# Kernel tuning notes

Hardware: AMD Instinct MI355X
Metric: run time of the kernel (lower is better)

The kernel has to match this reference:

```python
import jax, jax.numpy as jnp
import numpy as np

T, H, E, I = 16384, 2048, 16, 1408


def setup_inputs() -> dict:
    key = jax.random.key(0)
    k1, k2, k3, k4 = jax.random.split(key, 4)
    hidden_states = jax.random.normal(k1, (T, H), dtype=jnp.float32)
    router_logits = jax.random.normal(k2, (T, E), dtype=jnp.float32)
    # w13 = merged [gate; up] projection per expert: [E, 2*I, H] (w1 first, then w3)
    w13 = jax.random.normal(k3, (E, 2 * I, H), dtype=jnp.float32) * 0.02
    # w2 = down projection per expert: [E, H, I]
    w2 = jax.random.normal(k4, (E, H, I), dtype=jnp.float32) * 0.02
    return {
        "hidden_states": hidden_states,
        "router_logits": router_logits,
        "w13": w13,
        "w2": w2,
        "top_k": 2,
    }


def reference(hidden_states, router_logits, w13, w2, top_k):
    t, h = hidden_states.shape
    e = router_logits.shape[1]
    i = w2.shape[2]
    # softmax over experts, select top-k, renormalize selected weights
    probs = jax.nn.softmax(router_logits, axis=-1)                      # [T, E]
    topk_w, topk_ids = jax.lax.top_k(probs, top_k)                      # [T, K]
    topk_w = topk_w / jnp.sum(topk_w, axis=-1, keepdims=True)
    # dense combine weights, transposed to [E, T] for per-expert scan
    cw = jnp.zeros((t, e), probs.dtype).at[
        jnp.arange(t)[:, None], topk_ids
    ].add(topk_w).T                                                     # [E, T]

    def expert_step(out, inp):
        w13_e, w2_e, cw_e = inp                                         # [2I,H], [H,I], [T]
        g = hidden_states @ w13_e.T                                     # [T, 2I]
        act = jax.nn.silu(g[:, :i]) * g[:, i:]                          # SiLU-and-mul -> [T, I]
        y = act @ w2_e.T                                                # [T, H]
        return out + cw_e[:, None] * y, None

    out0 = jnp.zeros_like(hidden_states)
    out, _ = jax.lax.scan(expert_step, out0, (w13, w2, cw))
    return out
```

## Files before the change

kernel.cpp:

```cpp
#include <hip/hip_runtime.h>
#include <cstdio>
#include <cstdint>

#define T_TOK 16384
#define H_DIM 2048
#define E_NUM 16
#define I_DIM 1408
#define TWO_I 2816
#define PMAX  34816
#define MAXMT 272

typedef unsigned short ushort_t;
typedef __attribute__((ext_vector_type(8))) short bf16x8;
typedef __attribute__((ext_vector_type(4))) float f32x4;
typedef __attribute__((ext_vector_type(8))) unsigned short us8;

__device__ __forceinline__ ushort_t f2bf(float x) {
  union { float f; unsigned int u; } v; v.f = x;
  unsigned int r = v.u + 0x7fffu + ((v.u >> 16) & 1u);
  return (ushort_t)(r >> 16);
}

__device__ __forceinline__ float bf2f(ushort_t u) {
  union { unsigned int i; float f; } v; v.i = ((unsigned int)u) << 16; return v.f;
}

__device__ __forceinline__ void async_copy16(const void* g, void* l) {
  __builtin_amdgcn_global_load_lds(
      (const __attribute__((address_space(1))) unsigned int*)g,
      (__attribute__((address_space(3))) unsigned int*)l, 16, 0, 0);
}

__global__ void zero_small(int* counts, int* fill, int* ntl) {
  int i = threadIdx.x;
  if (i < E_NUM) { counts[i] = 0; fill[i] = 0; }
  if (i == 0) ntl[0] = 0;
}

__global__ void router_kernel(const float* __restrict__ logits,
                              int* __restrict__ tok_e, float* __restrict__ tok_w,
                              int* __restrict__ counts) {
  int t = blockIdx.x * 256 + threadIdx.x;
  if (t >= T_TOK) return;
  const float* lp = logits + (size_t)t * E_NUM;
  float b1 = -1e30f, b2 = -1e30f; int i1 = 0, i2 = 0;
#pragma unroll
  for (int e = 0; e < E_NUM; ++e) {
    float v = lp[e];
    if (v > b1) { b2 = b1; i2 = i1; b1 = v; i1 = e; }
    else if (v > b2) { b2 = v; i2 = e; }
  }
  float w1 = 1.f / (1.f + __expf(b2 - b1));
  tok_e[2 * t] = i1; tok_e[2 * t + 1] = i2;
  tok_w[2 * t] = w1; tok_w[2 * t + 1] = 1.f - w1;
  atomicAdd(&counts[i1], 1);
  atomicAdd(&counts[i2], 1);
}

__global__ void scan_kernel(const int* __restrict__ counts, int* __restrict__ base_e,
                            int* __restrict__ tile_expert, int* __restrict__ tile_base,
                            int* __restrict__ ntl) {
  if (threadIdx.x != 0) return;
  int base = 0, nt = 0;
  for (int e = 0; e < E_NUM; ++e) {
    base_e[e] = base;
    int c = counts[e];
    int tiles = (c + 127) >> 7;
    for (int ti = 0; ti < tiles; ++ti) { tile_expert[nt] = e; tile_base[nt] = base + ti * 128; ++nt; }
    base += tiles << 7;
  }
  ntl[0] = nt;
}

__global__ void slot_init_kernel(int* st, float* sw) {
  int i = blockIdx.x * 256 + threadIdx.x;
  if (i < PMAX) { st[i] = 0; sw[i] = 0.f; }
}

__global__ void scatter_kernel(const int* __restrict__ tok_e, const float* __restrict__ tok_w,
                               const int* __restrict__ base_e, int* __restrict__ fill,
                               int* __restrict__ st, float* __restrict__ sw,
                               int* __restrict__ tslot) {
  int t = blockIdx.x * 256 + threadIdx.x;
  if (t >= T_TOK) return;
#pragma unroll
  for (int k = 0; k < 2; ++k) {
    int e = tok_e[2 * t + k];
    int pos = atomicAdd(&fill[e], 1);
    int slot = base_e[e] + pos;
    st[slot] = t; sw[slot] = tok_w[2 * t + k];
    tslot[2 * t + k] = slot;
  }
}

__device__ __forceinline__ us8 pack8(float4 a, float4 b) {
  us8 r;
  r[0] = f2bf(a.x); r[1] = f2bf(a.y); r[2] = f2bf(a.z); r[3] = f2bf(a.w);
  r[4] = f2bf(b.x); r[5] = f2bf(b.y); r[6] = f2bf(b.z); r[7] = f2bf(b.w);
  return r;
}

__global__ void cvt_hidden(const float* __restrict__ src, ushort_t* __restrict__ dst) {
  size_t i8 = ((size_t)blockIdx.x * 256 + threadIdx.x) * 8;
  const float4* s = (const float4*)(src + i8);
  *(us8*)(dst + i8) = pack8(s[0], s[1]);
}

__global__ void cvt_w13(const float* __restrict__ src, ushort_t* __restrict__ dst) {
  size_t i8 = ((size_t)blockIdx.x * 256 + threadIdx.x) * 8;
  const size_t per_e = (size_t)TWO_I * H_DIM;
  int e = (int)(i8 / per_e);
  size_t rem = i8 - (size_t)e * per_e;
  int n = (int)(rem / H_DIM);
  int c = (int)(rem - (size_t)n * H_DIM);
  int np;
  if (n < I_DIM) np = ((n >> 4) << 5) + (n & 15);
  else { int m = n - I_DIM; np = ((m >> 4) << 5) + 16 + (m & 15); }
  const float4* s = (const float4*)(src + i8);
  *(us8*)(dst + (size_t)e * per_e + (size_t)np * H_DIM + c) = pack8(s[0], s[1]);
}

__global__ void cvt_w2(const float* __restrict__ src, ushort_t* __restrict__ dst) {
  size_t i8 = ((size_t)blockIdx.x * 256 + threadIdx.x) * 8;
  const float4* s = (const float4*)(src + i8);
  *(us8*)(dst + i8) = pack8(s[0], s[1]);
}

__global__ __launch_bounds__(256, 2) void gemm1_kernel(
    const ushort_t* __restrict__ Xb, const ushort_t* __restrict__ W13p,
    ushort_t* __restrict__ Act, const int* __restrict__ slot_token,
    const int* __restrict__ tile_expert, const int* __restrict__ tile_base,
    const int* __restrict__ ntl) {
  const int mt = blockIdx.y;
  if (mt >= ntl[0]) return;
  const int e = tile_expert[mt];
  const int slot0 = tile_base[mt];
  const int n0 = blockIdx.x * 128;

  __shared__ ushort_t As[128 * 64];
  __shared__ ushort_t Bs[128 * 64];
  __shared__ int toks[128];

  const int tid = threadIdx.x;
  if (tid < 128) toks[tid] = slot_token[slot0 + tid];
  __syncthreads();

  const int wave = tid >> 6;
  const int lane = tid & 63;
  const int r = lane & 15;
  const int q = lane >> 4;
  const int wm = wave >> 1;
  const int wn = wave & 1;

  const ushort_t* a_src[4];
  const ushort_t* b_src[4];
  ushort_t* a_dst[4];
  ushort_t* b_dst[4];
#pragma unroll
  for (int s = 0; s < 4; ++s) {
    int u = wave * 256 + s * 64 + lane;
    int m = u >> 3;
    int kc = (u & 7) ^ (m & 7);
    a_src[s] = Xb + (size_t)toks[m] * H_DIM + kc * 8;
    b_src[s] = W13p + (size_t)e * ((size_t)TWO_I * H_DIM) + (size_t)(n0 + m) * H_DIM + kc * 8;
    a_dst[s] = &As[(size_t)u * 8];
    b_dst[s] = &Bs[(size_t)u * 8];
  }

  int aoff[2][4], boff[2][4];
#pragma unroll
  for (int kh = 0; kh < 2; ++kh)
#pragma unroll
    for (int i = 0; i < 4; ++i) {
      int m = wm * 64 + i * 16 + r;
      aoff[kh][i] = (m * 8 + ((kh * 4 + q) ^ (r & 7))) * 8;
      int n = wn * 64 + i * 16 + r;
      boff[kh][i] = (n * 8 + ((kh * 4 + q) ^ (r & 7))) * 8;
    }

  f32x4 acc[4][4];
#pragma unroll
  for (int i = 0; i < 4; ++i)
#pragma unroll
    for (int j = 0; j < 4; ++j) acc[i][j] = (f32x4)(0.f);

  for (int kt = 0; kt < H_DIM / 64; ++kt) {
    const int koff = kt * 64;
#pragma unroll
    for (int s = 0; s < 4; ++s) {
      async_copy16(a_src[s] + koff, a_dst[s]);
      async_copy16(b_src[s] + koff, b_dst[s]);
    }
    __syncthreads();
#pragma unroll
    for (int kh = 0; kh < 2; ++kh) {
      bf16x8 af[4], bfr[4];
#pragma unroll
      for (int i = 0; i < 4; ++i) af[i] = *(const bf16x8*)&As[aoff[kh][i]];
#pragma unroll
      for (int j = 0; j < 4; ++j) bfr[j] = *(const bf16x8*)&Bs[boff[kh][j]];
#pragma unroll
      for (int i = 0; i < 4; ++i)
#pragma unroll
        for (int j = 0; j < 4; ++j)
          acc[i][j] = __builtin_amdgcn_mfma_f32_16x16x32_bf16(af[i], bfr[j], acc[i][j], 0, 0, 0);
    }
    __syncthreads();
  }

#pragma unroll
  for (int i = 0; i < 4; ++i) {
    const int row = slot0 + wm * 64 + i * 16 + q * 4;
#pragma unroll
    for (int jj = 0; jj < 2; ++jj) {
      const int g = 4 * (int)blockIdx.x + 2 * wn + jj;
      const int col = g * 16 + r;
      const f32x4 gv = acc[i][2 * jj];
      const f32x4 uv = acc[i][2 * jj + 1];
#pragma unroll
      for (int reg = 0; reg < 4; ++reg) {
        float gate = gv[reg];
        float a = gate / (1.f + __expf(-gate)) * uv[reg];
        Act[(size_t)(row + reg) * I_DIM + col] = f2bf(a);
      }
    }
  }
}

__global__ __launch_bounds__(256, 2) void gemm2_kernel(
    const ushort_t* __restrict__ Act, const ushort_t* __restrict__ W2b,
    ushort_t* __restrict__ Y, const float* __restrict__ slot_w,
    const int* __restrict__ tile_expert, const int* __restrict__ tile_base,
    const int* __restrict__ ntl) {
  const int mt = blockIdx.y;
  if (mt >= ntl[0]) return;
  const int e = tile_expert[mt];
  const int slot0 = tile_base[mt];
  const int n0 = blockIdx.x * 128;

  __shared__ ushort_t As[128 * 64];
  __shared__ ushort_t Bs[128 * 64];
  __shared__ float wgt[128];

  const int tid = threadIdx.x;
  if (tid < 128) wgt[tid] = slot_w[slot0 + tid];

  const int wave = tid >> 6;
  const int lane = tid & 63;
  const int r = lane & 15;
  const int q = lane >> 4;
  const int wm = wave >> 1;
  const int wn = wave & 1;

  const ushort_t* a_src[4];
  const ushort_t* b_src[4];
  ushort_t* a_dst[4];
  ushort_t* b_dst[4];
#pragma unroll
  for (int s = 0; s < 4; ++s) {
    int u = wave * 256 + s * 64 + lane;
    int m = u >> 3;
    int kc = (u & 7) ^ (m & 7);
    a_src[s] = Act + (size_t)(slot0 + m) * I_DIM + kc * 8;
    b_src[s] = W2b + (size_t)e * ((size_t)H_DIM * I_DIM) + (size_t)(n0 + m) * I_DIM + kc * 8;
    a_dst[s] = &As[(size_t)u * 8];
    b_dst[s] = &Bs[(size_t)u * 8];
  }

  int aoff[2][4], boff[2][4];
#pragma unroll
  for (int kh = 0; kh < 2; ++kh)
#pragma unroll
    for (int i = 0; i < 4; ++i) {
      int m = wm * 64 + i * 16 + r;
      aoff[kh][i] = (m * 8 + ((kh * 4 + q) ^ (r & 7))) * 8;
      int n = wn * 64 + i * 16 + r;
      boff[kh][i] = (n * 8 + ((kh * 4 + q) ^ (r & 7))) * 8;
    }

  f32x4 acc[4][4];
#pragma unroll
  for (int i = 0; i < 4; ++i)
#pragma unroll
    for (int j = 0; j < 4; ++j) acc[i][j] = (f32x4)(0.f);

  for (int kt = 0; kt < I_DIM / 64; ++kt) {
    const int koff = kt * 64;
#pragma unroll
    for (int s = 0; s < 4; ++s) {
      async_copy16(a_src[s] + koff, a_dst[s]);
      async_copy16(b_src[s] + koff, b_dst[s]);
    }
    __syncthreads();
#pragma unroll
    for (int kh = 0; kh < 2; ++kh) {
      bf16x8 af[4], bfr[4];
#pragma unroll
      for (int i = 0; i < 4; ++i) af[i] = *(const bf16x8*)&As[aoff[kh][i]];
#pragma unroll
      for (int j = 0; j < 4; ++j) bfr[j] = *(const bf16x8*)&Bs[boff[kh][j]];
#pragma unroll
      for (int i = 0; i < 4; ++i)
#pragma unroll
        for (int j = 0; j < 4; ++j)
          acc[i][j] = __builtin_amdgcn_mfma_f32_16x16x32_bf16(af[i], bfr[j], acc[i][j], 0, 0, 0);
    }
    __syncthreads();
  }

#pragma unroll
  for (int i = 0; i < 4; ++i) {
#pragma unroll
    for (int reg = 0; reg < 4; ++reg) {
      const int rl = wm * 64 + i * 16 + q * 4 + reg;
      const float w = wgt[rl];
      ushort_t* yrow = Y + (size_t)(slot0 + rl) * H_DIM;
#pragma unroll
      for (int j = 0; j < 4; ++j) {
        const int col = n0 + wn * 64 + j * 16 + r;
        yrow[col] = f2bf(w * acc[i][j][reg]);
      }
    }
  }
}

__global__ __launch_bounds__(256) void combine_kernel(
    const ushort_t* __restrict__ Y, const int* __restrict__ tslot,
    float* __restrict__ Out) {
  const int t = blockIdx.x;
  const int c = threadIdx.x * 8;
  const int s1 = tslot[2 * t];
  const int s2 = tslot[2 * t + 1];
  const us8 y1 = *(const us8*)(Y + (size_t)s1 * H_DIM + c);
  const us8 y2 = *(const us8*)(Y + (size_t)s2 * H_DIM + c);
  float4 o0, o1;
  o0.x = bf2f(y1[0]) + bf2f(y2[0]);
  o0.y = bf2f(y1[1]) + bf2f(y2[1]);
  o0.z = bf2f(y1[2]) + bf2f(y2[2]);
  o0.w = bf2f(y1[3]) + bf2f(y2[3]);
  o1.x = bf2f(y1[4]) + bf2f(y2[4]);
  o1.y = bf2f(y1[5]) + bf2f(y2[5]);
  o1.z = bf2f(y1[6]) + bf2f(y2[6]);
  o1.w = bf2f(y1[7]) + bf2f(y2[7]);
  float4* dst = (float4*)(Out + (size_t)t * H_DIM + c);
  dst[0] = o0;
  dst[1] = o1;
}

extern "C" void kernel_launch(void* const* d_in, const int* in_sizes, int n_in,
                              void* d_out, int out_size, void* d_ws, size_t ws_size,
                              hipStream_t stream) {
  const float* hidden = (const float*)d_in[0];
  const float* logits = (const float*)d_in[1];
  const float* w13    = (const float*)d_in[2];
  const float* w2     = (const float*)d_in[3];
  float* out = (float*)d_out;
  char* ws = (char*)d_ws;

  const size_t SZ_HID = (size_t)T_TOK * H_DIM * 2;
  const size_t SZ_W13 = (size_t)E_NUM * TWO_I * H_DIM * 2;
  const size_t SZ_W2  = (size_t)E_NUM * H_DIM * I_DIM * 2;
  const size_t SZ_Y   = (size_t)PMAX * H_DIM * 2;
  const size_t REGION0 = SZ_HID + SZ_W13;

  size_t off = 0;
  ushort_t* hid_b = (ushort_t*)(ws + off); off += SZ_HID;
  ushort_t* w13p  = (ushort_t*)(ws + off); off += SZ_W13;
  ushort_t* w2b   = (ushort_t*)ws;
  ushort_t* ybuf  = (ushort_t*)(ws + SZ_W2);
  ushort_t* act   = (ushort_t*)(ws + off); off += (size_t)PMAX * I_DIM * 2;
  int*   stok  = (int*)(ws + off);  off += (size_t)PMAX * 4;
  float* swt   = (float*)(ws + off); off += (size_t)PMAX * 4;
  int*   tok_e = (int*)(ws + off);  off += (size_t)T_TOK * 2 * 4;
  float* tok_w = (float*)(ws + off); off += (size_t)T_TOK * 2 * 4;
  int*   tslot = (int*)(ws + off);  off += (size_t)T_TOK * 2 * 4;
  int* counts = (int*)(ws + off); off += 256;
  int* fill   = (int*)(ws + off); off += 256;
  int* base_e = (int*)(ws + off); off += 256;
  int* texp   = (int*)(ws + off); off += MAXMT * 4;
  int* tbase  = (int*)(ws + off); off += MAXMT * 4;
  int* ntl    = (int*)(ws + off); off += 256;

  if (off > ws_size || SZ_W2 + SZ_Y > REGION0) {
    fprintf(stderr, "FusedMoE: ws too small: need %zu have %zu\n", off, ws_size);
    return;
  }

  zero_small<<<1, 64, 0, stream>>>(counts, fill, ntl);
  router_kernel<<<T_TOK / 256, 256, 0, stream>>>(logits, tok_e, tok_w, counts);
  scan_kernel<<<1, 64, 0, stream>>>(counts, base_e, texp, tbase, ntl);
  slot_init_kernel<<<(PMAX + 255) / 256, 256, 0, stream>>>(stok, swt);
  scatter_kernel<<<T_TOK / 256, 256, 0, stream>>>(tok_e, tok_w, base_e, fill, stok, swt, tslot);

  cvt_hidden<<<(T_TOK * H_DIM / 8) / 256, 256, 0, stream>>>(hidden, hid_b);
  cvt_w13<<<(unsigned)((size_t)E_NUM * TWO_I * H_DIM / 8 / 256), 256, 0, stream>>>(w13, w13p);

  dim3 g1(TWO_I / 128, MAXMT);
  gemm1_kernel<<<g1, 256, 0, stream>>>(hid_b, w13p, act, stok, texp, tbase, ntl);

  cvt_w2<<<(unsigned)((size_t)E_NUM * H_DIM * I_DIM / 8 / 256), 256, 0, stream>>>(w2, w2b);

  dim3 g2(H_DIM / 128, MAXMT);
  gemm2_kernel<<<g2, 256, 0, stream>>>(act, w2b, ybuf, swt, texp, tbase, ntl);

  combine_kernel<<<T_TOK, 256, 0, stream>>>(ybuf, tslot, out);
}
```

Before: 1.676 ms.

## Enlarge MoE GEMM tiles to 256x256 with double-buffered LDS pipeline

Both grouped GEMMs move from 128x128 tiles with 4 waves to 256x256 tiles with 8 waves. They double-buffer LDS so the next K-slice's async loads overlap MFMA work, and use explicit waitcnt/barrier phases with s_setprio around the MFMA bursts. Blocks are launched as a 1D grid with an XCD-aware swizzle, and the routing scan becomes a wave-parallel prefix with 256-row expert padding. The larger tiles raise arithmetic intensity and cut global traffic, at the cost of more padding rows per expert, higher register pressure and LDS use, and possibly lower occupancy.

```diff
diff --git a/kernel.cpp b/kernel.cpp
--- a/kernel.cpp
+++ b/kernel.cpp
@@ -7,8 +7,12 @@
 #define E_NUM 16
 #define I_DIM 1408
 #define TWO_I 2816
-#define PMAX  34816
-#define MAXMT 272
+#define BM    256
+#define BK    64
+#define PMAX  36864
+#define MAXMT 144
+#define NX1   11
+#define NX2   8
 
 typedef unsigned short ushort_t;
 typedef __attribute__((ext_vector_type(8))) short bf16x8;
@@ -58,18 +62,21 @@
 }
 
 __global__ void scan_kernel(const int* __restrict__ counts, int* __restrict__ base_e,
-                            int* __restrict__ tile_expert, int* __restrict__ tile_base,
-                            int* __restrict__ ntl) {
-  if (threadIdx.x != 0) return;
-  int base = 0, nt = 0;
-  for (int e = 0; e < E_NUM; ++e) {
-    base_e[e] = base;
-    int c = counts[e];
-    int tiles = (c + 127) >> 7;
-    for (int ti = 0; ti < tiles; ++ti) { tile_expert[nt] = e; tile_base[nt] = base + ti * 128; ++nt; }
-    base += tiles << 7;
-  }
-  ntl[0] = nt;
+                            int* __restrict__ tile_expert, int* __restrict__ ntl) {
+  int lane = threadIdx.x;
+  int c = (lane < E_NUM) ? counts[lane] : 0;
+  int tiles = (c + 255) >> 8;
+  int pre = 0;
+#pragma unroll
+  for (int k = 0; k < E_NUM; ++k) {
+    int tk = __shfl(tiles, k, 64);
+    if (k < lane) pre += tk;
+  }
+  if (lane < E_NUM) {
+    base_e[lane] = pre << 8;
+    for (int ti = 0; ti < tiles; ++ti) tile_expert[pre + ti] = lane;
+    if (lane == E_NUM - 1) ntl[0] = pre + tiles;
+  }
 }
 
 __global__ void slot_init_kernel(int* st, float* sw) {
@@ -126,94 +133,178 @@
   *(us8*)(dst + i8) = pack8(s[0], s[1]);
 }
 
-__global__ __launch_bounds__(256, 2) void gemm1_kernel(
+
+__global__ __launch_bounds__(512, 2) void gemm1_kernel(
     const ushort_t* __restrict__ Xb, const ushort_t* __restrict__ W13p,
     ushort_t* __restrict__ Act, const int* __restrict__ slot_token,
-    const int* __restrict__ tile_expert, const int* __restrict__ tile_base,
-    const int* __restrict__ ntl) {
-  const int mt = blockIdx.y;
+    const int* __restrict__ tile_expert, const int* __restrict__ ntl) {
+  const int bid = blockIdx.x;
+  const int wg = (bid & 7) * (NX1 * MAXMT / 8) + (bid >> 3);
+  const int mt = wg / NX1;
+  const int nb = wg - mt * NX1;
   if (mt >= ntl[0]) return;
   const int e = tile_expert[mt];
-  const int slot0 = tile_base[mt];
-  const int n0 = blockIdx.x * 128;
-
-  __shared__ ushort_t As[128 * 64];
-  __shared__ ushort_t Bs[128 * 64];
-  __shared__ int toks[128];
+  const int slot0 = mt * BM;
+  const int n0 = nb * BM;
+
+  __shared__ ushort_t As[2][BM * BK];
+  __shared__ ushort_t Bs[2][BM * BK];
+  __shared__ int toks[BM];
 
   const int tid = threadIdx.x;
-  if (tid < 128) toks[tid] = slot_token[slot0 + tid];
+  if (tid < BM) toks[tid] = slot_token[slot0 + tid];
   __syncthreads();
 
   const int wave = tid >> 6;
   const int lane = tid & 63;
   const int r = lane & 15;
   const int q = lane >> 4;
-  const int wm = wave >> 1;
-  const int wn = wave & 1;
+  const int wm = wave >> 2;
+  const int wn = wave & 3;
 
   const ushort_t* a_src[4];
   const ushort_t* b_src[4];
-  ushort_t* a_dst[4];
-  ushort_t* b_dst[4];
+  int dst_u[4];
 #pragma unroll
   for (int s = 0; s < 4; ++s) {
-    int u = wave * 256 + s * 64 + lane;
+    int u = s * 512 + tid;
     int m = u >> 3;
     int kc = (u & 7) ^ (m & 7);
     a_src[s] = Xb + (size_t)toks[m] * H_DIM + kc * 8;
     b_src[s] = W13p + (size_t)e * ((size_t)TWO_I * H_DIM) + (size_t)(n0 + m) * H_DIM + kc * 8;
-    a_dst[s] = &As[(size_t)u * 8];
-    b_dst[s] = &Bs[(size_t)u * 8];
-  }
-
-  int aoff[2][4], boff[2][4];
-#pragma unroll
-  for (int kh = 0; kh < 2; ++kh)
-#pragma unroll
-    for (int i = 0; i < 4; ++i) {
-      int m = wm * 64 + i * 16 + r;
-      aoff[kh][i] = (m * 8 + ((kh * 4 + q) ^ (r & 7))) * 8;
-      int n = wn * 64 + i * 16 + r;
-      boff[kh][i] = (n * 8 + ((kh * 4 + q) ^ (r & 7))) * 8;
-    }
-
-  f32x4 acc[4][4];
-#pragma unroll
-  for (int i = 0; i < 4; ++i)
+    dst_u[s] = u * 8;
+  }
+
+  int aoff[8], boff[4];
+#pragma unroll
+  for (int i = 0; i < 8; ++i) {
+    int m = wm * 128 + i * 16 + r;
+    aoff[i] = (m * 8 + (q ^ (m & 7))) * 8;
+  }
+#pragma unroll
+  for (int j = 0; j < 4; ++j) {
+    int n = wn * 64 + j * 16 + r;
+    boff[j] = (n * 8 + (q ^ (n & 7))) * 8;
+  }
+
+  f32x4 acc[8][4];
+#pragma unroll
+  for (int i = 0; i < 8; ++i)
 #pragma unroll
     for (int j = 0; j < 4; ++j) acc[i][j] = (f32x4)(0.f);
 
-  for (int kt = 0; kt < H_DIM / 64; ++kt) {
-    const int koff = kt * 64;
-#pragma unroll
-    for (int s = 0; s < 4; ++s) {
-      async_copy16(a_src[s] + koff, a_dst[s]);
-      async_copy16(b_src[s] + koff, b_dst[s]);
-    }
-    __syncthreads();
-#pragma unroll
-    for (int kh = 0; kh < 2; ++kh) {
-      bf16x8 af[4], bfr[4];
-#pragma unroll
-      for (int i = 0; i < 4; ++i) af[i] = *(const bf16x8*)&As[aoff[kh][i]];
-#pragma unroll
-      for (int j = 0; j < 4; ++j) bfr[j] = *(const bf16x8*)&Bs[boff[kh][j]];
-#pragma unroll
-      for (int i = 0; i < 4; ++i)
-#pragma unroll
-        for (int j = 0; j < 4; ++j)
-          acc[i][j] = __builtin_amdgcn_mfma_f32_16x16x32_bf16(af[i], bfr[j], acc[i][j], 0, 0, 0);
-    }
-    __syncthreads();
-  }
-
-#pragma unroll
-  for (int i = 0; i < 4; ++i) {
-    const int row = slot0 + wm * 64 + i * 16 + q * 4;
-#pragma unroll
-    for (int jj = 0; jj < 2; ++jj) {
-      const int g = 4 * (int)blockIdx.x + 2 * wn + jj;
+  const int NT = H_DIM / BK;
+
+#pragma unroll
+  for (int s = 0; s < 4; ++s) {
+    async_copy16(a_src[s], &As[0][dst_u[s]]);
+    async_copy16(b_src[s], &Bs[0][dst_u[s]]);
+  }
+
+  for (int t = 0; t < NT; ++t) {
+    const int cur = t & 1;
+    const int nxt = cur ^ 1;
+    if (t + 1 < NT) {
+      const int koff = (t + 1) * BK;
+#pragma unroll
+      for (int s = 0; s < 4; ++s) {
+        async_copy16(a_src[s] + koff, &As[nxt][dst_u[s]]);
+        async_copy16(b_src[s] + koff, &Bs[nxt][dst_u[s]]);
+      }
+      asm volatile("s_waitcnt vmcnt(8)" ::: "memory");
+    } else {
+      asm volatile("s_waitcnt vmcnt(0)" ::: "memory");
+    }
+    __builtin_amdgcn_s_barrier();
+
+    const ushort_t* A = &As[cur][0];
+    const ushort_t* B = &Bs[cur][0];
+    bf16x8 af[4][2], bfr[2][2];
+
+#pragma unroll
+    for (int ii = 0; ii < 4; ++ii) {
+      af[ii][0] = *(const bf16x8*)&A[aoff[ii]];
+      af[ii][1] = *(const bf16x8*)&A[aoff[ii] ^ 32];
+    }
+#pragma unroll
+    for (int jj = 0; jj < 2; ++jj) {
+      bfr[jj][0] = *(const bf16x8*)&B[boff[jj]];
+      bfr[jj][1] = *(const bf16x8*)&B[boff[jj] ^ 32];
+    }
+    __builtin_amdgcn_s_barrier();
+    asm volatile("s_waitcnt lgkmcnt(0)" ::: "memory");
+    __builtin_amdgcn_s_setprio(1);
+#pragma unroll
+    for (int ii = 0; ii < 4; ++ii)
+#pragma unroll
+      for (int jj = 0; jj < 2; ++jj) {
+        acc[ii][jj] = __builtin_amdgcn_mfma_f32_16x16x32_bf16(af[ii][0], bfr[jj][0], acc[ii][jj], 0, 0, 0);
+        acc[ii][jj] = __builtin_amdgcn_mfma_f32_16x16x32_bf16(af[ii][1], bfr[jj][1], acc[ii][jj], 0, 0, 0);
+      }
+    __builtin_amdgcn_s_setprio(0);
+    __builtin_amdgcn_s_barrier();
+
+#pragma unroll
+    for (int jj = 0; jj < 2; ++jj) {
+      bfr[jj][0] = *(const bf16x8*)&B[boff[2 + jj]];
+      bfr[jj][1] = *(const bf16x8*)&B[boff[2 + jj] ^ 32];
+    }
+    __builtin_amdgcn_s_barrier();
+    asm volatile("s_waitcnt lgkmcnt(0)" ::: "memory");
+    __builtin_amdgcn_s_setprio(1);
+#pragma unroll
+    for (int ii = 0; ii < 4; ++ii)
+#pragma unroll
+      for (int jj = 0; jj < 2; ++jj) {
+        acc[ii][2 + jj] = __builtin_amdgcn_mfma_f32_16x16x32_bf16(af[ii][0], bfr[jj][0], acc[ii][2 + jj], 0, 0, 0);
+        acc[ii][2 + jj] = __builtin_amdgcn_mfma_f32_16x16x32_bf16(af[ii][1], bfr[jj][1], acc[ii][2 + jj], 0, 0, 0);
+      }
+    __builtin_amdgcn_s_setprio(0);
+    __builtin_amdgcn_s_barrier();
+
+#pragma unroll
+    for (int ii = 0; ii < 4; ++ii) {
+      af[ii][0] = *(const bf16x8*)&A[aoff[4 + ii]];
+      af[ii][1] = *(const bf16x8*)&A[aoff[4 + ii] ^ 32];
+    }
+    __builtin_amdgcn_s_barrier();
+    asm volatile("s_waitcnt lgkmcnt(0)" ::: "memory");
+    __builtin_amdgcn_s_setprio(1);
+#pragma unroll
+    for (int ii = 0; ii < 4; ++ii)
+#pragma unroll
+      for (int jj = 0; jj < 2; ++jj) {
+        acc[4 + ii][2 + jj] = __builtin_amdgcn_mfma_f32_16x16x32_bf16(af[ii][0], bfr[jj][0], acc[4 + ii][2 + jj], 0, 0, 0);
+        acc[4 + ii][2 + jj] = __builtin_amdgcn_mfma_f32_16x16x32_bf16(af[ii][1], bfr[jj][1], acc[4 + ii][2 + jj], 0, 0, 0);
+      }
+    __builtin_amdgcn_s_setprio(0);
+    __builtin_amdgcn_s_barrier();
+
+#pragma unroll
+    for (int jj = 0; jj < 2; ++jj) {
+      bfr[jj][0] = *(const bf16x8*)&B[boff[jj]];
+      bfr[jj][1] = *(const bf16x8*)&B[boff[jj] ^ 32];
+    }
+    __builtin_amdgcn_s_barrier();
+    asm volatile("s_waitcnt lgkmcnt(0)" ::: "memory");
+    __builtin_amdgcn_s_setprio(1);
+#pragma unroll
+    for (int ii = 0; ii < 4; ++ii)
+#pragma unroll
+      for (int jj = 0; jj < 2; ++jj) {
+        acc[4 + ii][jj] = __builtin_amdgcn_mfma_f32_16x16x32_bf16(af[ii][0], bfr[jj][0], acc[4 + ii][jj], 0, 0, 0);
+        acc[4 + ii][jj] = __builtin_amdgcn_mfma_f32_16x16x32_bf16(af[ii][1], bfr[jj][1], acc[4 + ii][jj], 0, 0, 0);
+      }
+    __builtin_amdgcn_s_setprio(0);
+    __builtin_amdgcn_s_barrier();
+  }
+
+#pragma unroll
+  for (int i = 0; i < 8; ++i) {
+    const int row = slot0 + wm * 128 + i * 16 + q * 4;
+#pragma unroll
+    for (int jj = 0; jj < 2; ++jj) {
+      const int g = nb * 8 + wn * 2 + jj;
       const int col = g * 16 + r;
       const f32x4 gv = acc[i][2 * jj];
       const f32x4 uv = acc[i][2 * jj + 1];
@@ -227,99 +318,180 @@
   }
 }
 
-__global__ __launch_bounds__(256, 2) void gemm2_kernel(
+__global__ __launch_bounds__(512, 2) void gemm2_kernel(
     const ushort_t* __restrict__ Act, const ushort_t* __restrict__ W2b,
     ushort_t* __restrict__ Y, const float* __restrict__ slot_w,
-    const int* __restrict__ tile_expert, const int* __restrict__ tile_base,
-    const int* __restrict__ ntl) {
-  const int mt = blockIdx.y;
+    const int* __restrict__ tile_expert, const int* __restrict__ ntl) {
+  const int bid = blockIdx.x;
+  const int wg = (bid & 7) * (NX2 * MAXMT / 8) + (bid >> 3);
+  const int mt = wg >> 3;
+  const int nb = wg & 7;
   if (mt >= ntl[0]) return;
   const int e = tile_expert[mt];
-  const int slot0 = tile_base[mt];
-  const int n0 = blockIdx.x * 128;
-
-  __shared__ ushort_t As[128 * 64];
-  __shared__ ushort_t Bs[128 * 64];
-  __shared__ float wgt[128];
+  const int slot0 = mt * BM;
+  const int n0 = nb * BM;
+
+  __shared__ ushort_t As[2][BM * BK];
+  __shared__ ushort_t Bs[2][BM * BK];
+  __shared__ float wgt[BM];
 
   const int tid = threadIdx.x;
-  if (tid < 128) wgt[tid] = slot_w[slot0 + tid];
+  if (tid < BM) wgt[tid] = slot_w[slot0 + tid];
+  __syncthreads();
 
   const int wave = tid >> 6;
   const int lane = tid & 63;
   const int r = lane & 15;
   const int q = lane >> 4;
-  const int wm = wave >> 1;
-  const int wn = wave & 1;
+  const int wm = wave >> 2;
+  const int wn = wave & 3;
 
   const ushort_t* a_src[4];
   const ushort_t* b_src[4];
-  ushort_t* a_dst[4];
-  ushort_t* b_dst[4];
+  int dst_u[4];
 #pragma unroll
   for (int s = 0; s < 4; ++s) {
-    int u = wave * 256 + s * 64 + lane;
+    int u = s * 512 + tid;
     int m = u >> 3;
     int kc = (u & 7) ^ (m & 7);
     a_src[s] = Act + (size_t)(slot0 + m) * I_DIM + kc * 8;
     b_src[s] = W2b + (size_t)e * ((size_t)H_DIM * I_DIM) + (size_t)(n0 + m) * I_DIM + kc * 8;
-    a_dst[s] = &As[(size_t)u * 8];
-    b_dst[s] = &Bs[(size_t)u * 8];
-  }
-
-  int aoff[2][4], boff[2][4];
-#pragma unroll
-  for (int kh = 0; kh < 2; ++kh)
-#pragma unroll
-    for (int i = 0; i < 4; ++i) {
-      int m = wm * 64 + i * 16 + r;
-      aoff[kh][i] = (m * 8 + ((kh * 4 + q) ^ (r & 7))) * 8;
-      int n = wn * 64 + i * 16 + r;
-      boff[kh][i] = (n * 8 + ((kh * 4 + q) ^ (r & 7))) * 8;
-    }
-
-  f32x4 acc[4][4];
-#pragma unroll
-  for (int i = 0; i < 4; ++i)
+    dst_u[s] = u * 8;
+  }
+
+  int aoff[8], boff[4];
+#pragma unroll
+  for (int i = 0; i < 8; ++i) {
+    int m = wm * 128 + i * 16 + r;
+    aoff[i] = (m * 8 + (q ^ (m & 7))) * 8;
+  }
+#pragma unroll
+  for (int j = 0; j < 4; ++j) {
+    int n = wn * 64 + j * 16 + r;
+    boff[j] = (n * 8 + (q ^ (n & 7))) * 8;
+  }
+
+  f32x4 acc[8][4];
+#pragma unroll
+  for (int i = 0; i < 8; ++i)
 #pragma unroll
     for (int j = 0; j < 4; ++j) acc[i][j] = (f32x4)(0.f);
 
-  for (int kt = 0; kt < I_DIM / 64; ++kt) {
-    const int koff = kt * 64;
-#pragma unroll
-    for (int s = 0; s < 4; ++s) {
-      async_copy16(a_src[s] + koff, a_dst[s]);
-      async_copy16(b_src[s] + koff, b_dst[s]);
-    }
-    __syncthreads();
-#pragma unroll
-    for (int kh = 0; kh < 2; ++kh) {
-      bf16x8 af[4], bfr[4];
-#pragma unroll
-      for (int i = 0; i < 4; ++i) af[i] = *(const bf16x8*)&As[aoff[kh][i]];
-#pragma unroll
-      for (int j = 0; j < 4; ++j) bfr[j] = *(const bf16x8*)&Bs[boff[kh][j]];
-#pragma unroll
-      for (int i = 0; i < 4; ++i)
-#pragma unroll
-        for (int j = 0; j < 4; ++j)
-          acc[i][j] = __builtin_amdgcn_mfma_f32_16x16x32_bf16(af[i], bfr[j], acc[i][j], 0, 0, 0);
-    }
-    __syncthreads();
-  }
-
-#pragma unroll
-  for (int i = 0; i < 4; ++i) {
+  const int NT = I_DIM / BK;
+
+#pragma unroll
+  for (int s = 0; s < 4; ++s) {
+    async_copy16(a_src[s], &As[0][dst_u[s]]);
+    async_copy16(b_src[s], &Bs[0][dst_u[s]]);
+  }
+
+  for (int t = 0; t < NT; ++t) {
+    const int cur = t & 1;
+    const int nxt = cur ^ 1;
+    if (t + 1 < NT) {
+      const int koff = (t + 1) * BK;
+#pragma unroll
+      for (int s = 0; s < 4; ++s) {
+        async_copy16(a_src[s] + koff, &As[nxt][dst_u[s]]);
+        async_copy16(b_src[s] + koff, &Bs[nxt][dst_u[s]]);
+      }
+      asm volatile("s_waitcnt vmcnt(8)" ::: "memory");
+    } else {
+      asm volatile("s_waitcnt vmcnt(0)" ::: "memory");
+    }
+    __builtin_amdgcn_s_barrier();
+
+    const ushort_t* A = &As[cur][0];
+    const ushort_t* B = &Bs[cur][0];
+    bf16x8 af[4][2], bfr[2][2];
+
+#pragma unroll
+    for (int ii = 0; ii < 4; ++ii) {
+      af[ii][0] = *(const bf16x8*)&A[aoff[ii]];
+      af[ii][1] = *(const bf16x8*)&A[aoff[ii] ^ 32];
+    }
+#pragma unroll
+    for (int jj = 0; jj < 2; ++jj) {
+      bfr[jj][0] = *(const bf16x8*)&B[boff[jj]];
+      bfr[jj][1] = *(const bf16x8*)&B[boff[jj] ^ 32];
+    }
+    __builtin_amdgcn_s_barrier();
+    asm volatile("s_waitcnt lgkmcnt(0)" ::: "memory");
+    __builtin_amdgcn_s_setprio(1);
+#pragma unroll
+    for (int ii = 0; ii < 4; ++ii)
+#pragma unroll
+      for (int jj = 0; jj < 2; ++jj) {
+        acc[ii][jj] = __builtin_amdgcn_mfma_f32_16x16x32_bf16(af[ii][0], bfr[jj][0], acc[ii][jj], 0, 0, 0);
+        acc[ii][jj] = __builtin_amdgcn_mfma_f32_16x16x32_bf16(af[ii][1], bfr[jj][1], acc[ii][jj], 0, 0, 0);
+      }
+    __builtin_amdgcn_s_setprio(0);
+    __builtin_amdgcn_s_barrier();
+
+#pragma unroll
+    for (int jj = 0; jj < 2; ++jj) {
+      bfr[jj][0] = *(const bf16x8*)&B[boff[2 + jj]];
+      bfr[jj][1] = *(const bf16x8*)&B[boff[2 + jj] ^ 32];
+    }
+    __builtin_amdgcn_s_barrier();
+    asm volatile("s_waitcnt lgkmcnt(0)" ::: "memory");
+    __builtin_amdgcn_s_setprio(1);
+#pragma unroll
+    for (int ii = 0; ii < 4; ++ii)
+#pragma unroll
+      for (int jj = 0; jj < 2; ++jj) {
+        acc[ii][2 + jj] = __builtin_amdgcn_mfma_f32_16x16x32_bf16(af[ii][0], bfr[jj][0], acc[ii][2 + jj], 0, 0, 0);
+        acc[ii][2 + jj] = __builtin_amdgcn_mfma_f32_16x16x32_bf16(af[ii][1], bfr[jj][1], acc[ii][2 + jj], 0, 0, 0);
+      }
+    __builtin_amdgcn_s_setprio(0);
+    __builtin_amdgcn_s_barrier();
+
+#pragma unroll
+    for (int ii = 0; ii < 4; ++ii) {
+      af[ii][0] = *(const bf16x8*)&A[aoff[4 + ii]];
+      af[ii][1] = *(const bf16x8*)&A[aoff[4 + ii] ^ 32];
+    }
+    __builtin_amdgcn_s_barrier();
+    asm volatile("s_waitcnt lgkmcnt(0)" ::: "memory");
+    __builtin_amdgcn_s_setprio(1);
+#pragma unroll
+    for (int ii = 0; ii < 4; ++ii)
+#pragma unroll
+      for (int jj = 0; jj < 2; ++jj) {
+        acc[4 + ii][2 + jj] = __builtin_amdgcn_mfma_f32_16x16x32_bf16(af[ii][0], bfr[jj][0], acc[4 + ii][2 + jj], 0, 0, 0);
+        acc[4 + ii][2 + jj] = __builtin_amdgcn_mfma_f32_16x16x32_bf16(af[ii][1], bfr[jj][1], acc[4 + ii][2 + jj], 0, 0, 0);
+      }
+    __builtin_amdgcn_s_setprio(0);
+    __builtin_amdgcn_s_barrier();
+
+#pragma unroll
+    for (int jj = 0; jj < 2; ++jj) {
+      bfr[jj][0] = *(const bf16x8*)&B[boff[jj]];
+      bfr[jj][1] = *(const bf16x8*)&B[boff[jj] ^ 32];
+    }
+    __builtin_amdgcn_s_barrier();
+    asm volatile("s_waitcnt lgkmcnt(0)" ::: "memory");
+    __builtin_amdgcn_s_setprio(1);
+#pragma unroll
+    for (int ii = 0; ii < 4; ++ii)
+#pragma unroll
+      for (int jj = 0; jj < 2; ++jj) {
+        acc[4 + ii][jj] = __builtin_amdgcn_mfma_f32_16x16x32_bf16(af[ii][0], bfr[jj][0], acc[4 + ii][jj], 0, 0, 0);
+        acc[4 + ii][jj] = __builtin_amdgcn_mfma_f32_16x16x32_bf16(af[ii][1], bfr[jj][1], acc[4 + ii][jj], 0, 0, 0);
+      }
+    __builtin_amdgcn_s_setprio(0);
+    __builtin_amdgcn_s_barrier();
+  }
+
+#pragma unroll
+  for (int i = 0; i < 8; ++i) {
 #pragma unroll
     for (int reg = 0; reg < 4; ++reg) {
-      const int rl = wm * 64 + i * 16 + q * 4 + reg;
+      const int rl = wm * 128 + i * 16 + q * 4 + reg;
       const float w = wgt[rl];
-      ushort_t* yrow = Y + (size_t)(slot0 + rl) * H_DIM;
-#pragma unroll
-      for (int j = 0; j < 4; ++j) {
-        const int col = n0 + wn * 64 + j * 16 + r;
-        yrow[col] = f2bf(w * acc[i][j][reg]);
-      }
+      ushort_t* yrow = Y + (size_t)(slot0 + rl) * H_DIM + n0 + wn * 64;
+#pragma unroll
+      for (int j = 0; j < 4; ++j) yrow[j * 16 + r] = f2bf(w * acc[i][j][reg]);
     }
   }
 }
@@ -378,7 +550,6 @@
   int* fill   = (int*)(ws + off); off += 256;
   int* base_e = (int*)(ws + off); off += 256;
   int* texp   = (int*)(ws + off); off += MAXMT * 4;
-  int* tbase  = (int*)(ws + off); off += MAXMT * 4;
   int* ntl    = (int*)(ws + off); off += 256;
 
   if (off > ws_size || SZ_W2 + SZ_Y > REGION0) {
@@ -388,20 +559,18 @@
 
   zero_small<<<1, 64, 0, stream>>>(counts, fill, ntl);
   router_kernel<<<T_TOK / 256, 256, 0, stream>>>(logits, tok_e, tok_w, counts);
-  scan_kernel<<<1, 64, 0, stream>>>(counts, base_e, texp, tbase, ntl);
+  scan_kernel<<<1, 64, 0, stream>>>(counts, base_e, texp, ntl);
   slot_init_kernel<<<(PMAX + 255) / 256, 256, 0, stream>>>(stok, swt);
   scatter_kernel<<<T_TOK / 256, 256, 0, stream>>>(tok_e, tok_w, base_e, fill, stok, swt, tslot);
 
   cvt_hidden<<<(T_TOK * H_DIM / 8) / 256, 256, 0, stream>>>(hidden, hid_b);
   cvt_w13<<<(unsigned)((size_t)E_NUM * TWO_I * H_DIM / 8 / 256), 256, 0, stream>>>(w13, w13p);
 
-  dim3 g1(TWO_I / 128, MAXMT);
-  gemm1_kernel<<<g1, 256, 0, stream>>>(hid_b, w13p, act, stok, texp, tbase, ntl);
+  gemm1_kernel<<<NX1 * MAXMT, 512, 0, stream>>>(hid_b, w13p, act, stok, texp, ntl);
 
   cvt_w2<<<(unsigned)((size_t)E_NUM * H_DIM * I_DIM / 8 / 256), 256, 0, stream>>>(w2, w2b);
 
-  dim3 g2(H_DIM / 128, MAXMT);
-  gemm2_kernel<<<g2, 256, 0, stream>>>(act, w2b, ybuf, swt, texp, tbase, ntl);
+  gemm2_kernel<<<NX2 * MAXMT, 512, 0, stream>>>(act, w2b, ybuf, swt, texp, ntl);
 
   combine_kernel<<<T_TOK, 256, 0, stream>>>(ybuf, tslot, out);
 }
```

New measurement: 1.904 ms. 13.6% more time.

## Remap GEMM workgroups across XCDs, parallelize tile scan, simplify conversion indexing

Applied to the files above, without the earlier changes.

Both grouped GEMMs move from a 2D grid to a 1D grid whose block id is remapped so that consecutive workgroups on the same XCD (bid & 7 interleave) share the same N-block and walk adjacent M tiles. The aim is better L2 reuse of expert weight tiles within each XCD. The tile scan becomes a wave-parallel prefix sum over experts and drops the tile_base array, since slot0 = mt*128. The router loads logits as float4, and cvt_w13 uses a 2D grid to avoid 64-bit divisions.

```diff
diff --git a/kernel.cpp b/kernel.cpp
--- a/kernel.cpp
+++ b/kernel.cpp
@@ -9,6 +9,8 @@
 #define TWO_I 2816
 #define PMAX  34816
 #define MAXMT 272
+#define NX1   22
+#define NX2   16
 
 typedef unsigned short ushort_t;
 typedef __attribute__((ext_vector_type(8))) short bf16x8;
@@ -42,11 +44,14 @@
                               int* __restrict__ counts) {
   int t = blockIdx.x * 256 + threadIdx.x;
   if (t >= T_TOK) return;
-  const float* lp = logits + (size_t)t * E_NUM;
+  const float4* lp = (const float4*)(logits + (size_t)t * E_NUM);
+  float4 v0 = lp[0], v1 = lp[1], v2 = lp[2], v3 = lp[3];
+  float a[16] = {v0.x, v0.y, v0.z, v0.w, v1.x, v1.y, v1.z, v1.w,
+                 v2.x, v2.y, v2.z, v2.w, v3.x, v3.y, v3.z, v3.w};
   float b1 = -1e30f, b2 = -1e30f; int i1 = 0, i2 = 0;
 #pragma unroll
   for (int e = 0; e < E_NUM; ++e) {
-    float v = lp[e];
+    float v = a[e];
     if (v > b1) { b2 = b1; i2 = i1; b1 = v; i1 = e; }
     else if (v > b2) { b2 = v; i2 = e; }
   }
@@ -58,18 +63,21 @@
 }
 
 __global__ void scan_kernel(const int* __restrict__ counts, int* __restrict__ base_e,
-                            int* __restrict__ tile_expert, int* __restrict__ tile_base,
-                            int* __restrict__ ntl) {
-  if (threadIdx.x != 0) return;
-  int base = 0, nt = 0;
-  for (int e = 0; e < E_NUM; ++e) {
-    base_e[e] = base;
-    int c = counts[e];
-    int tiles = (c + 127) >> 7;
-    for (int ti = 0; ti < tiles; ++ti) { tile_expert[nt] = e; tile_base[nt] = base + ti * 128; ++nt; }
-    base += tiles << 7;
-  }
-  ntl[0] = nt;
+                            int* __restrict__ tile_expert, int* __restrict__ ntl) {
+  int lane = threadIdx.x;
+  int c = (lane < E_NUM) ? counts[lane] : 0;
+  int tiles = (c + 127) >> 7;
+  int pre = 0;
+#pragma unroll
+  for (int k = 0; k < E_NUM; ++k) {
+    int tk = __shfl(tiles, k, 64);
+    if (k < lane) pre += tk;
+  }
+  if (lane < E_NUM) {
+    base_e[lane] = pre << 7;
+    for (int ti = 0; ti < tiles; ++ti) tile_expert[pre + ti] = lane;
+    if (lane == E_NUM - 1) ntl[0] = pre + tiles;
+  }
 }
 
 __global__ void slot_init_kernel(int* st, float* sw) {
@@ -107,16 +115,14 @@
 }
 
 __global__ void cvt_w13(const float* __restrict__ src, ushort_t* __restrict__ dst) {
-  size_t i8 = ((size_t)blockIdx.x * 256 + threadIdx.x) * 8;
-  const size_t per_e = (size_t)TWO_I * H_DIM;
-  int e = (int)(i8 / per_e);
-  size_t rem = i8 - (size_t)e * per_e;
-  int n = (int)(rem / H_DIM);
-  int c = (int)(rem - (size_t)n * H_DIM);
+  const int n = blockIdx.x;
+  const int e = blockIdx.y;
+  const int c = threadIdx.x * 8;
   int np;
   if (n < I_DIM) np = ((n >> 4) << 5) + (n & 15);
   else { int m = n - I_DIM; np = ((m >> 4) << 5) + 16 + (m & 15); }
-  const float4* s = (const float4*)(src + i8);
+  const size_t per_e = (size_t)TWO_I * H_DIM;
+  const float4* s = (const float4*)(src + (size_t)e * per_e + (size_t)n * H_DIM + c);
   *(us8*)(dst + (size_t)e * per_e + (size_t)np * H_DIM + c) = pack8(s[0], s[1]);
 }
 
@@ -129,13 +135,16 @@
 __global__ __launch_bounds__(256, 2) void gemm1_kernel(
     const ushort_t* __restrict__ Xb, const ushort_t* __restrict__ W13p,
     ushort_t* __restrict__ Act, const int* __restrict__ slot_token,
-    const int* __restrict__ tile_expert, const int* __restrict__ tile_base,
-    const int* __restrict__ ntl) {
-  const int mt = blockIdx.y;
+    const int* __restrict__ tile_expert, const int* __restrict__ ntl) {
+  const int CH = NX1 * MAXMT / 8;
+  const int bid = blockIdx.x;
+  const int wg = (bid & 7) * CH + (bid >> 3);
+  const int mt = wg % MAXMT;
+  const int nb = wg / MAXMT;
   if (mt >= ntl[0]) return;
   const int e = tile_expert[mt];
-  const int slot0 = tile_base[mt];
-  const int n0 = blockIdx.x * 128;
+  const int slot0 = mt * 128;
+  const int n0 = nb * 128;
 
   __shared__ ushort_t As[128 * 64];
   __shared__ ushort_t Bs[128 * 64];
@@ -213,7 +222,7 @@
     const int row = slot0 + wm * 64 + i * 16 + q * 4;
 #pragma unroll
     for (int jj = 0; jj < 2; ++jj) {
-      const int g = 4 * (int)blockIdx.x + 2 * wn + jj;
+      const int g = 4 * nb + 2 * wn + jj;
       const int col = g * 16 + r;
       const f32x4 gv = acc[i][2 * jj];
       const f32x4 uv = acc[i][2 * jj + 1];
@@ -230,13 +239,16 @@
 __global__ __launch_bounds__(256, 2) void gemm2_kernel(
     const ushort_t* __restrict__ Act, const ushort_t* __restrict__ W2b,
     ushort_t* __restrict__ Y, const float* __restrict__ slot_w,
-    const int* __restrict__ tile_expert, const int* __restrict__ tile_base,
-    const int* __restrict__ ntl) {
-  const int mt = blockIdx.y;
+    const int* __restrict__ tile_expert, const int* __restrict__ ntl) {
+  const int CH = NX2 * MAXMT / 8;
+  const int bid = blockIdx.x;
+  const int wg = (bid & 7) * CH + (bid >> 3);
+  const int mt = wg % MAXMT;
+  const int nb = wg / MAXMT;
   if (mt >= ntl[0]) return;
   const int e = tile_expert[mt];
-  const int slot0 = tile_base[mt];
-  const int n0 = blockIdx.x * 128;
+  const int slot0 = mt * 128;
+  const int n0 = nb * 128;
 
   __shared__ ushort_t As[128 * 64];
   __shared__ ushort_t Bs[128 * 64];
@@ -378,7 +390,6 @@
   int* fill   = (int*)(ws + off); off += 256;
   int* base_e = (int*)(ws + off); off += 256;
   int* texp   = (int*)(ws + off); off += MAXMT * 4;
-  int* tbase  = (int*)(ws + off); off += MAXMT * 4;
   int* ntl    = (int*)(ws + off); off += 256;
 
   if (off > ws_size || SZ_W2 + SZ_Y > REGION0) {
@@ -388,20 +399,21 @@
 
   zero_small<<<1, 64, 0, stream>>>(counts, fill, ntl);
   router_kernel<<<T_TOK / 256, 256, 0, stream>>>(logits, tok_e, tok_w, counts);
-  scan_kernel<<<1, 64, 0, stream>>>(counts, base_e, texp, tbase, ntl);
+  scan_kernel<<<1, 64, 0, stream>>>(counts, base_e, texp, ntl);
   slot_init_kernel<<<(PMAX + 255) / 256, 256, 0, stream>>>(stok, swt);
   scatter_kernel<<<T_TOK / 256, 256, 0, stream>>>(tok_e, tok_w, base_e, fill, stok, swt, tslot);
 
   cvt_hidden<<<(T_TOK * H_DIM / 8) / 256, 256, 0, stream>>>(hidden, hid_b);
-  cvt_w13<<<(unsigned)((size_t)E_NUM * TWO_I * H_DIM / 8 / 256), 256, 0, stream>>>(w13, w13p);
-
-  dim3 g1(TWO_I / 128, MAXMT);
-  gemm1_kernel<<<g1, 256, 0, stream>>>(hid_b, w13p, act, stok, texp, tbase, ntl);
+  {
+    dim3 gw13(TWO_I, E_NUM);
+    cvt_w13<<<gw13, 256, 0, stream>>>(w13, w13p);
+  }
+
+  gemm1_kernel<<<NX1 * MAXMT, 256, 0, stream>>>(hid_b, w13p, act, stok, texp, ntl);
 
   cvt_w2<<<(unsigned)((size_t)E_NUM * H_DIM * I_DIM / 8 / 256), 256, 0, stream>>>(w2, w2b);
 
-  dim3 g2(H_DIM / 128, MAXMT);
-  gemm2_kernel<<<g2, 256, 0, stream>>>(act, w2b, ybuf, swt, texp, tbase, ntl);
+  gemm2_kernel<<<NX2 * MAXMT, 256, 0, stream>>>(act, w2b, ybuf, swt, texp, ntl);
 
   combine_kernel<<<T_TOK, 256, 0, stream>>>(ybuf, tslot, out);
 }
```

Measured after the change: 1.653 ms. No clear change (-1.4%).
